# Performance work log

Measured on AMD Instinct MI355X. Metric: run time of the kernel, lower is better.

Reference implementation:

```python
import jax, jax.numpy as jnp
import numpy as np

R, K, CF, HF, WF = 64, 81, 256, 256, 256  # ROIs, classes(incl bg), FPN channels, P2 size
IMG = 1024.0
SCALE = 0.25          # P2 feature stride 4
STEPS = 4             # subdivision steps: 7 -> 112
NPTS = 28 * 28        # subdivision_num_points
FC = 256


def _grid_sample(img, coords):
    """torch.grid_sample(bilinear, align_corners=False, zeros padding).
    img: [N,C,H,W]; coords: [N,P,2] (x,y) in [0,1]. Returns [N,C,P]."""
    N, C, H, W = img.shape
    x = coords[..., 0] * W - 0.5
    y = coords[..., 1] * H - 0.5
    x0 = jnp.floor(x); y0 = jnp.floor(y)
    fx = x - x0; fy = y - y0

    def g(ix, iy, w):
        valid = (ix >= 0) & (ix < W) & (iy >= 0) & (iy < H)
        ixc = jnp.clip(ix, 0, W - 1).astype(jnp.int32)
        iyc = jnp.clip(iy, 0, H - 1).astype(jnp.int32)
        v = jax.vmap(lambda im, yy, xx: im[:, yy, xx])(img, iyc, ixc)  # [N,C,P]
        return v * (w * valid)[:, None, :]

    return (g(x0, y0, (1 - fx) * (1 - fy)) + g(x0 + 1, y0, fx * (1 - fy))
            + g(x0, y0 + 1, (1 - fx) * fy) + g(x0 + 1, y0 + 1, fx * fy))


def _point_head(fine, coarse, W1, b1, W2, b2, W3, b3, Wp, bp):
    # StandardPointHead: 1x1-conv fc layers, coarse logits re-concatenated each layer
    x = jnp.concatenate([fine, coarse], axis=1)  # [R, CF+K, P]
    for Wl, bl in ((W1, b1), (W2, b2), (W3, b3)):
        x = jax.nn.relu(jnp.einsum('oc,rcp->rop', Wl, x) + bl[None, :, None])
        x = jnp.concatenate([x, coarse], axis=1)
    return jnp.einsum('oc,rcp->rop', Wp, x) + bp[None, :, None]  # [R,K,P]


def setup_inputs() -> dict:
    key = jax.random.key(0)
    ks = jax.random.split(key, 12)
    feat = jax.random.normal(ks[0], (1, CF, HF, WF), dtype=jnp.float32)
    u = jax.random.uniform(ks[1], (R, 4), dtype=jnp.float32)
    x0 = u[:, 0] * (IMG - 256.0); y0 = u[:, 1] * (IMG - 256.0)
    w = 32.0 + u[:, 2] * 224.0;   h = 32.0 + u[:, 3] * 224.0
    det_bboxes = jnp.stack([x0, y0, x0 + w, y0 + h], axis=1)
    det_labels = jax.random.randint(ks[2], (R,), 0, 80, dtype=jnp.int32)
    coarse_logits = jax.random.normal(ks[3], (R, K, 7, 7), dtype=jnp.float32)
    cin = CF + K  # = FC + K = 337 for all layers here
    s = 0.02
    return {
        'feat': feat, 'det_bboxes': det_bboxes, 'det_labels': det_labels,
        'coarse_logits': coarse_logits,
        'W1': jax.random.normal(ks[4], (FC, cin), jnp.float32) * s,
        'b1': jnp.zeros((FC,), jnp.float32),
        'W2': jax.random.normal(ks[5], (FC, FC + K), jnp.float32) * s,
        'b2': jnp.zeros((FC,), jnp.float32),
        'W3': jax.random.normal(ks[6], (FC, FC + K), jnp.float32) * s,
        'b3': jnp.zeros((FC,), jnp.float32),
        'Wp': jax.random.normal(ks[7], (K, FC + K), jnp.float32) * s,
        'bp': jnp.zeros((K,), jnp.float32),
    }


def reference(feat, det_bboxes, det_labels, coarse_logits,
              W1, b1, W2, b2, W3, b3, Wp, bp):
    ml = coarse_logits
    bx0, by0 = det_bboxes[:, 0], det_bboxes[:, 1]
    bw = det_bboxes[:, 2] - det_bboxes[:, 0]
    bh = det_bboxes[:, 3] - det_bboxes[:, 1]
    for step in range(STEPS):
        _, _, H, W = ml.shape
        H, W = 2 * H, 2 * W
        # bilinear x2, align_corners=False (half-pixel centers)
        ml = jax.image.resize(ml, (R, K, H, W), method='linear')
        if NPTS >= 4 * H * W and step < STEPS - 1:
            continue
        # uncertainty = -|logit of gt class| (det_labels+1 skips background ch 0)
        gt = ml[jnp.arange(R), det_labels + 1]              # [R,H,W]
        unc = -jnp.abs(gt).reshape(R, H * W)
        _, idx = jax.lax.top_k(unc, NPTS)                   # [R,NPTS]
        px = ((idx % W).astype(ml.dtype) + 0.5) / W
        py = ((idx // W).astype(ml.dtype) + 0.5) / H
        coords = jnp.stack([px, py], axis=-1)               # [R,NPTS,2] in ROI [0,1]
        # project ROI coords to image, then to P2 normalized coords
        cx = bx0[:, None] + coords[..., 0] * bw[:, None]
        cy = by0[:, None] + coords[..., 1] * bh[:, None]
        fcoords = jnp.stack([cx * SCALE / WF, cy * SCALE / HF], axis=-1)
        fine = _grid_sample(feat, fcoords.reshape(1, R * NPTS, 2))  # [1,CF,R*NPTS]
        fine = fine[0].reshape(CF, R, NPTS).transpose(1, 0, 2)      # [R,CF,NPTS]
        coarse = _grid_sample(coarse_logits, coords)                # [R,K,NPTS]
        pl = _point_head(fine, coarse, W1, b1, W2, b2, W3, b3, Wp, bp)
        ml = jax.vmap(lambda m, i, p: m.at[:, i].set(p))(
            ml.reshape(R, K, H * W), idx, pl).reshape(R, K, H, W)
    return ml
```

## Files before the change

kernel.cpp:

```cpp
#include <hip/hip_runtime.h>
#include <hip/hip_bf16.h>
#include <cstdint>
#include <cstddef>

#define R_ 64
#define K_ 81
#define NPTS_ 784

typedef __attribute__((ext_vector_type(8))) short short8;
typedef __attribute__((ext_vector_type(4))) float f32x4;

#define GLDS16(G, L)                                                           \
  __builtin_amdgcn_global_load_lds(                                            \
      (__attribute__((address_space(1))) void*)(void*)(G),                     \
      (__attribute__((address_space(3))) void*)(L), 16, 0, 0)

__global__ __launch_bounds__(256) void transpose_feat_kernel(const float* __restrict__ in,
                                                             float* __restrict__ out) {
  __shared__ float tile[32][33];
  int y = blockIdx.z;
  int x0 = blockIdx.x * 32, c0 = blockIdx.y * 32;
  int tx = threadIdx.x, ty = threadIdx.y;
#pragma unroll
  for (int j = 0; j < 32; j += 8)
    tile[ty + j][tx] = in[(size_t)(c0 + ty + j) * 65536 + (size_t)y * 256 + x0 + tx];
  __syncthreads();
#pragma unroll
  for (int j = 0; j < 32; j += 8)
    out[((size_t)y * 256 + (x0 + ty + j)) * 256 + c0 + tx] = tile[tx][ty + j];
}

__global__ void prep_all_kernel(const float* __restrict__ W1, const float* __restrict__ W2,
                                const float* __restrict__ W3, const float* __restrict__ Wp,
                                const float* __restrict__ b1, const float* __restrict__ b2,
                                const float* __restrict__ b3, const float* __restrict__ bp,
                                const float* __restrict__ coarse_in,
                                __hip_bfloat16* __restrict__ Wpk, float* __restrict__ bias_all,
                                float* __restrict__ coarseT) {
  int t = blockIdx.x * 256 + threadIdx.x;
  if (t < 90112) {
    int lane = t & 63;
    int t2 = t >> 6;
    int hl = t2 & 1;
    t2 >>= 1;
    int jg = t2 & 15;
    t2 >>= 4;
    int kt = t2 % 11;
    int L = t2 / 11;
    int o = jg * 16 + (lane & 15);
    int kbase = kt * 32 + (lane >> 4) * 8;
    const float* Wsrc = (L == 0) ? W1 : (L == 1) ? W2 : (L == 2) ? W3 : Wp;
    int Omax = (L == 3) ? 81 : 256;
    __hip_bfloat16 outv[8];
#pragma unroll
    for (int e = 0; e < 8; ++e) {
      int k = kbase + e;
      float v = (o < Omax && k < 337) ? Wsrc[o * 337 + k] : 0.f;
      __hip_bfloat16 h = __float2bfloat16(v);
      outv[e] = hl ? __float2bfloat16(v - __bfloat162float(h)) : h;
    }
    *(short8*)(Wpk + (size_t)t * 8) = *(const short8*)outv;
  } else if (t < 90112 + 1024) {
    int k = t - 90112;
    float v = 0.f;
    if (k < 256) v = b1[k];
    else if (k < 512) v = b2[k - 256];
    else if (k < 768) v = b3[k - 512];
    else if (k < 768 + 81) v = bp[k - 768];
    bias_all[k] = v;
  } else {
    int t2 = t - 91136;
    if (t2 < R_ * 49 * K_) {
      int k = t2 % K_;
      int t3 = t2 / K_;
      int pos = t3 % 49;
      int r = t3 / 49;
      coarseT[t2] = coarse_in[((size_t)r * K_ + k) * 49 + pos];
    }
  }
}

__global__ __launch_bounds__(128) void upsample2x_kernel(const float* __restrict__ in,
                                                         float* __restrict__ out,
                                                         int Hin, int Win) {
  int b = blockIdx.z;
  int iy = blockIdx.y * 2 + threadIdx.y;
  int ix = blockIdx.x * 64 + threadIdx.x;
  if (ix >= Win || iy >= Hin) return;
  const float* p = in + (size_t)b * Hin * Win;
  int rT = (iy == 0) ? 0 : iy - 1;
  int rB = (iy == Hin - 1) ? iy : iy + 1;
  int cL = (ix == 0) ? 0 : ix - 1;
  int cR = (ix == Win - 1) ? ix : ix + 1;
  float wyT1 = (iy == 0) ? 0.f : 0.75f;
  float wyB1 = (iy == Hin - 1) ? 0.f : 0.25f;
  float wxE1 = (ix == 0) ? 0.f : 0.75f;
  float wxO1 = (ix == Win - 1) ? 0.f : 0.25f;
  float wyT0 = 1.f - wyT1, wyB0 = 1.f - wyB1;
  float wxE0 = 1.f - wxE1, wxO0 = 1.f - wxO1;

  const float* rowA = p + (size_t)rT * Win;
  const float* rowM = p + (size_t)iy * Win;
  const float* rowC = p + (size_t)rB * Win;
  float al = rowA[cL], am = rowA[ix], ar = rowA[cR];
  float mL = rowM[cL], mm = rowM[ix], mr = rowM[cR];
  float cl = rowC[cL], cm = rowC[ix], cr = rowC[cR];

  float aE = wxE0 * al + wxE1 * am;
  float aO = wxO0 * am + wxO1 * ar;
  float mE = wxE0 * mL + wxE1 * mm;
  float mO = wxO0 * mm + wxO1 * mr;
  float cE = wxE0 * cl + wxE1 * cm;
  float cO = wxO0 * cm + wxO1 * cr;

  float oTE = wyT0 * aE + wyT1 * mE;
  float oTO = wyT0 * aO + wyT1 * mO;
  float oBE = wyB0 * mE + wyB1 * cE;
  float oBO = wyB0 * mO + wyB1 * cO;

  int Wout = 2 * Win;
  float* ob = out + ((size_t)b * (2 * Hin) + 2 * iy) * Wout + 2 * ix;
  *(float2*)ob = make_float2(oTE, oTO);
  *(float2*)(ob + Wout) = make_float2(oBE, oBO);
}

__global__ __launch_bounds__(1024) void topk_kernel(const float* __restrict__ ml,
                                                    const int* __restrict__ labels,
                                                    int N, int* __restrict__ sel) {
  int r = blockIdx.x;
  const float* gt = ml + ((size_t)r * K_ + (labels[r] + 1)) * N;
  __shared__ unsigned int hist[256];
  __shared__ unsigned int sh_prefix, sh_remaining, sh_countless;
  __shared__ unsigned int wtot_less[16], wtot_eq[16];
  const int tid = threadIdx.x;
  const int lane = tid & 63;
  const int wv = tid >> 6;

  unsigned int prefix = 0;
  unsigned int remaining = NPTS_;
  unsigned int count_less = 0;
  for (int pass = 0; pass < 4; ++pass) {
    int shift = 24 - 8 * pass;
    if (tid < 256) hist[tid] = 0;
    __syncthreads();
    for (int i = tid; i < N; i += 1024) {
      unsigned int v = __float_as_uint(fabsf(gt[i]));
      bool match = (pass == 0) || ((v >> (shift + 8)) == prefix);
      unsigned int dg = (v >> shift) & 255u;
      if (pass == 0) {
        bool active = match;
        while (true) {
          unsigned long long act = __ballot(active);
          if (!act) break;
          int leader = (int)(__ffsll((long long)act) - 1);
          unsigned int ld = __shfl(dg, leader);
          bool same = active && (dg == ld);
          unsigned long long sm = __ballot(same);
          if (lane == leader) atomicAdd(&hist[ld], (unsigned int)__popcll(sm));
          active = active && !same;
        }
      } else if (match) {
        atomicAdd(&hist[dg], 1u);
      }
    }
    __syncthreads();
    if (tid < 64) {
      unsigned int s0 = hist[4 * lane + 0], s1 = hist[4 * lane + 1];
      unsigned int s2 = hist[4 * lane + 2], s3 = hist[4 * lane + 3];
      unsigned int ls = s0 + s1 + s2 + s3;
      unsigned int inc = ls;
#pragma unroll
      for (int d = 1; d < 64; d <<= 1) {
        unsigned int tv = __shfl_up(inc, d);
        if (lane >= d) inc += tv;
      }
      unsigned int exc = inc - ls;
      bool cross = (exc < remaining) && (exc + ls >= remaining);
      if (cross) {
        unsigned int before = exc;
        int d = 4 * lane;
        if (before + s0 < remaining) {
          before += s0; d++;
          if (before + s1 < remaining) {
            before += s1; d++;
            if (before + s2 < remaining) { before += s2; d++; }
          }
        }
        sh_prefix = (prefix << 8) | (unsigned int)d;
        sh_remaining = remaining - before;
        sh_countless = count_less + before;
      }
    }
    __syncthreads();
    prefix = sh_prefix;
    remaining = sh_remaining;
    count_less = sh_countless;
    __syncthreads();
  }
  unsigned int vstar = prefix;
  unsigned int need_eq = NPTS_ - count_less;

  unsigned int base_less = 0, base_eq = 0;
  int* selr = sel + (size_t)r * NPTS_;
  for (int base = 0; base < N; base += 1024) {
    int i = base + tid;
    bool less = false, eq = false;
    if (i < N) {
      unsigned int v = __float_as_uint(fabsf(gt[i]));
      less = v < vstar;
      eq = v == vstar;
    }
    unsigned long long ml_ = __ballot(less);
    unsigned long long me_ = __ballot(eq);
    unsigned long long lanemask = (lane == 0) ? 0ull : ((~0ull) >> (64 - lane));
    unsigned int pl = __popcll(ml_ & lanemask);
    unsigned int pe = __popcll(me_ & lanemask);
    if (lane == 0) {
      wtot_less[wv] = (unsigned int)__popcll(ml_);
      wtot_eq[wv] = (unsigned int)__popcll(me_);
    }
    __syncthreads();
    unsigned int off_l = 0, off_e = 0, tot_l = 0, tot_e = 0;
#pragma unroll
    for (int w2 = 0; w2 < 16; ++w2) {
      unsigned int tl = wtot_less[w2], te = wtot_eq[w2];
      if (w2 < wv) { off_l += tl; off_e += te; }
      tot_l += tl;
      tot_e += te;
    }
    if (less) selr[base_less + off_l + pl] = i;
    if (eq) {
      unsigned int er = base_eq + off_e + pe;
      if (er < need_eq) selr[count_less + er] = i;
    }
    base_less += tot_l;
    base_eq += tot_e;
    __syncthreads();
  }
}

__global__ __launch_bounds__(256) void sample_kernel(const int* __restrict__ sel,
                                                     const float* __restrict__ bboxes,
                                                     const float* __restrict__ featT,
                                                     const float* __restrict__ coarseT,
                                                     __hip_bfloat16* __restrict__ Xh,
                                                     __hip_bfloat16* __restrict__ Xl,
                                                     __hip_bfloat16* __restrict__ Cth,
                                                     __hip_bfloat16* __restrict__ Ctl,
                                                     int Wlev, int Hlev) {
  int rp = blockIdx.x;
  int r = rp / NPTS_;
  int idx = sel ? sel[rp] : (rp % NPTS_);
  int tid = threadIdx.x;

  float px = ((float)(idx % Wlev) + 0.5f) / (float)Wlev;
  float py = ((float)(idx / Wlev) + 0.5f) / (float)Hlev;
  float bx0 = bboxes[r * 4 + 0], by0 = bboxes[r * 4 + 1];
  float bw = __fsub_rn(bboxes[r * 4 + 2], bx0);
  float bh = __fsub_rn(bboxes[r * 4 + 3], by0);
  float cx = __fadd_rn(bx0, __fmul_rn(px, bw));
  float cy = __fadd_rn(by0, __fmul_rn(py, bh));

  {
    float gx = __fsub_rn(__fmul_rn(cx, 0.25f), 0.5f);
    float gy = __fsub_rn(__fmul_rn(cy, 0.25f), 0.5f);
    float fxf = floorf(gx), fyf = floorf(gy);
    float fx = __fsub_rn(gx, fxf), fy = __fsub_rn(gy, fyf);
    int x0 = (int)fxf, y0 = (int)fyf;
    float ofx = __fsub_rn(1.f, fx), ofy = __fsub_rn(1.f, fy);
    float w00 = __fmul_rn(ofx, ofy);
    float w10 = __fmul_rn(fx, ofy);
    float w01 = __fmul_rn(ofx, fy);
    float w11 = __fmul_rn(fx, fy);
    bool vx0 = (x0 >= 0) && (x0 < 256), vx1 = (x0 + 1 >= 0) && (x0 + 1 < 256);
    bool vy0 = (y0 >= 0) && (y0 < 256), vy1 = (y0 + 1 >= 0) && (y0 + 1 < 256);
    float W00 = (vx0 && vy0) ? w00 : 0.f;
    float W10 = (vx1 && vy0) ? w10 : 0.f;
    float W01 = (vx0 && vy1) ? w01 : 0.f;
    float W11 = (vx1 && vy1) ? w11 : 0.f;
    int x0c = min(max(x0, 0), 255), x1c = min(max(x0 + 1, 0), 255);
    int y0c = min(max(y0, 0), 255), y1c = min(max(y0 + 1, 0), 255);
    const float* p00 = featT + ((size_t)(y0c * 256 + x0c)) * 256;
    const float* p10 = featT + ((size_t)(y0c * 256 + x1c)) * 256;
    const float* p01 = featT + ((size_t)(y1c * 256 + x0c)) * 256;
    const float* p11 = featT + ((size_t)(y1c * 256 + x1c)) * 256;
    float acc = __fmul_rn(p00[tid], W00);
    acc = __fadd_rn(acc, __fmul_rn(p10[tid], W10));
    acc = __fadd_rn(acc, __fmul_rn(p01[tid], W01));
    acc = __fadd_rn(acc, __fmul_rn(p11[tid], W11));
    __hip_bfloat16 h = __float2bfloat16(acc);
    Xh[(size_t)rp * 256 + tid] = h;
    Xl[(size_t)rp * 256 + tid] = __float2bfloat16(acc - __bfloat162float(h));
  }

  if (tid < 96) {
    float acc = 0.f;
    if (tid < K_) {
      float gx = __fsub_rn(__fmul_rn(px, 7.f), 0.5f);
      float gy = __fsub_rn(__fmul_rn(py, 7.f), 0.5f);
      float fxf = floorf(gx), fyf = floorf(gy);
      float fx = __fsub_rn(gx, fxf), fy = __fsub_rn(gy, fyf);
      int x0 = (int)fxf, y0 = (int)fyf;
      float ofx = __fsub_rn(1.f, fx), ofy = __fsub_rn(1.f, fy);
      float w00 = __fmul_rn(ofx, ofy);
      float w10 = __fmul_rn(fx, ofy);
      float w01 = __fmul_rn(ofx, fy);
      float w11 = __fmul_rn(fx, fy);
      bool vx0 = (x0 >= 0) && (x0 < 7), vx1 = (x0 + 1 >= 0) && (x0 + 1 < 7);
      bool vy0 = (y0 >= 0) && (y0 < 7), vy1 = (y0 + 1 >= 0) && (y0 + 1 < 7);
      float W00 = (vx0 && vy0) ? w00 : 0.f;
      float W10 = (vx1 && vy0) ? w10 : 0.f;
      float W01 = (vx0 && vy1) ? w01 : 0.f;
      float W11 = (vx1 && vy1) ? w11 : 0.f;
      int x0c = min(max(x0, 0), 6), x1c = min(max(x0 + 1, 0), 6);
      int y0c = min(max(y0, 0), 6), y1c = min(max(y0 + 1, 0), 6);
      const float* cb = coarseT + (size_t)r * 49 * K_;
      acc = __fmul_rn(cb[(size_t)(y0c * 7 + x0c) * K_ + tid], W00);
      acc = __fadd_rn(acc, __fmul_rn(cb[(size_t)(y0c * 7 + x1c) * K_ + tid], W10));
      acc = __fadd_rn(acc, __fmul_rn(cb[(size_t)(y1c * 7 + x0c) * K_ + tid], W01));
      acc = __fadd_rn(acc, __fmul_rn(cb[(size_t)(y1c * 7 + x1c) * K_ + tid], W11));
    }
    __hip_bfloat16 h = __float2bfloat16(acc);
    Cth[(size_t)rp * 96 + tid] = h;
    Ctl[(size_t)rp * 96 + tid] = __float2bfloat16(acc - __bfloat162float(h));
  }
}

template <int TERMS>
__global__ __launch_bounds__(256, 2) void fused_head_kernel(
    const __hip_bfloat16* __restrict__ Ah, const __hip_bfloat16* __restrict__ Al,
    const __hip_bfloat16* __restrict__ Th, const __hip_bfloat16* __restrict__ Tl,
    const __hip_bfloat16* __restrict__ Wpk,
    const float* __restrict__ bias_all, float* __restrict__ PL) {
  constexpr int XPLANE = 11 * 4096;
  constexpr int XLO = 8 * 4096;
  __shared__ char lds[(TERMS == 3) ? XPLANE + XLO : XPLANE];
  char* Xh = lds;
  char* Xl = lds + XPLANE;

  const int tid = threadIdx.x;
  const int lane = tid & 63;
  const int w = tid >> 6;
  const int g = lane >> 4;
  const int lane15 = lane & 15;
  const int m0 = blockIdx.x * 64;

  {
    const int srow = tid >> 2;
    const int sp = tid & 3;
    const int sx = sp ^ ((srow >> 1) & 3);
#pragma unroll
    for (int kt = 0; kt < 8; ++kt) {
      size_t off = (((size_t)(m0 + srow)) * 256 + (size_t)kt * 32 + (size_t)sx * 8) * 2;
      GLDS16((const char*)Ah + off, Xh + kt * 4096 + w * 1024);
      if constexpr (TERMS == 3) GLDS16((const char*)Al + off, Xl + kt * 4096 + w * 1024);
    }
#pragma unroll
    for (int kt = 8; kt < 11; ++kt) {
      size_t off = (((size_t)(m0 + srow)) * 96 + (size_t)(kt - 8) * 32 + (size_t)sx * 8) * 2;
      GLDS16((const char*)Th + off, Xh + kt * 4096 + w * 1024);
    }
  }
  asm volatile("s_waitcnt vmcnt(0)" ::: "memory");
  __syncthreads();

  int offA[4];
#pragma unroll
  for (int i = 0; i < 4; ++i) {
    int rowA = i * 16 + lane15;
    offA[i] = rowA * 64 + ((g ^ ((rowA >> 1) & 3)) << 4);
  }

#pragma unroll 1
  for (int L = 0; L < 4; ++L) {
    if (L == 3 && w >= 2) break;
    const __hip_bfloat16* WL = Wpk + (size_t)L * (11 * 16 * 2 * 512);

    f32x4 acc[4][4];
#pragma unroll
    for (int i = 0; i < 4; ++i)
#pragma unroll
      for (int j = 0; j < 4; ++j) acc[i][j] = (f32x4){0.f, 0.f, 0.f, 0.f};

    short8 a_h[4], a_l[4], b_h[2][4], b_l[2][4], tl_buf[2][4];

    auto loadB = [&](int buf, int kt) {
#pragma unroll
      for (int j = 0; j < 4; ++j) {
        const __hip_bfloat16* bp =
            WL + (((size_t)kt * 16 + (w * 4 + j)) * 2) * 512 + (size_t)lane * 8;
        b_h[buf][j] = *(const short8*)bp;
        if constexpr (TERMS == 3) b_l[buf][j] = *(const short8*)(bp + 512);
      }
    };
    auto loadTl = [&](int buf, int kt) {
#pragma unroll
      for (int i = 0; i < 4; ++i)
        tl_buf[buf][i] = *(const short8*)((const char*)Tl +
            (((size_t)(m0 + i * 16 + lane15)) * 96 + (size_t)(kt - 8) * 32 +
             (size_t)g * 8) * 2);
    };

    loadB(0, 0);

#pragma unroll
    for (int kt = 0; kt < 11; ++kt) {
      const int cb = kt & 1;
      if (kt < 10) {
        loadB(cb ^ 1, kt + 1);
        if constexpr (TERMS == 3) {
          if (kt + 1 >= 8) loadTl((kt + 1) & 1, kt + 1);
        }
      }
      __builtin_amdgcn_sched_barrier(0);
#pragma unroll
      for (int i = 0; i < 4; ++i) {
        a_h[i] = *(const short8*)(Xh + kt * 4096 + offA[i]);
        if constexpr (TERMS == 3) {
          if (kt < 8)
            a_l[i] = *(const short8*)(Xl + kt * 4096 + offA[i]);
          else
            a_l[i] = tl_buf[kt & 1][i];
        }
      }
      __builtin_amdgcn_s_setprio(1);
#pragma unroll
      for (int i = 0; i < 4; ++i)
#pragma unroll
        for (int j = 0; j < 4; ++j) {
          acc[i][j] = __builtin_amdgcn_mfma_f32_16x16x32_bf16(a_h[i], b_h[cb][j], acc[i][j], 0, 0, 0);
          if constexpr (TERMS == 3) {
            acc[i][j] = __builtin_amdgcn_mfma_f32_16x16x32_bf16(a_h[i], b_l[cb][j], acc[i][j], 0, 0, 0);
            acc[i][j] = __builtin_amdgcn_mfma_f32_16x16x32_bf16(a_l[i], b_h[cb][j], acc[i][j], 0, 0, 0);
          }
        }
      __builtin_amdgcn_s_setprio(0);
      __builtin_amdgcn_sched_barrier(0);
    }

    if (L < 3) {
      __syncthreads();
#pragma unroll
      for (int j = 0; j < 4; ++j) {
        int o = w * 64 + j * 16 + lane15;
        float bv = bias_all[L * 256 + o];
        int kch = o >> 5;
        int s0 = (o >> 3) & 3;
        int e = o & 7;
#pragma unroll
        for (int i = 0; i < 4; ++i) {
          int mb = i * 16 + g * 4;
#pragma unroll
          for (int r = 0; r < 4; ++r) {
            int m = mb + r;
            float v = fmaxf(acc[i][j][r] + bv, 0.f);
            __hip_bfloat16 h = __float2bfloat16(v);
            int boff = kch * 4096 + m * 64 + ((s0 ^ ((m >> 1) & 3)) << 4) + e * 2;
            *(__hip_bfloat16*)(Xh + boff) = h;
            if constexpr (TERMS == 3)
              *(__hip_bfloat16*)(Xl + boff) = __float2bfloat16(v - __bfloat162float(h));
          }
        }
      }
      __syncthreads();
    } else {
#pragma unroll
      for (int j = 0; j < 4; ++j) {
        int o = w * 64 + j * 16 + lane15;
        float bv = bias_all[768 + o];
#pragma unroll
        for (int i = 0; i < 4; ++i) {
          int mb = i * 16 + g * 4;
#pragma unroll
          for (int r = 0; r < 4; ++r)
            PL[(size_t)(m0 + mb + r) * 128 + o] = acc[i][j][r] + bv;
        }
      }
    }
  }
}

__global__ void scatter_kernel(const float* __restrict__ PL, const int* __restrict__ sel,
                               float* __restrict__ ml, int Nlev) {
  int t = blockIdx.x * 256 + threadIdx.x;
  if (t >= R_ * NPTS_ * K_) return;
  int k = t % K_;
  int rp = t / K_;
  int i = sel ? sel[rp] : (rp % NPTS_);
  int r = rp / NPTS_;
  ml[((size_t)r * K_ + k) * Nlev + i] = PL[(size_t)rp * 128 + k];
}

extern "C" void kernel_launch(void* const* d_in, const int* in_sizes, int n_in,
                              void* d_out, int out_size, void* d_ws, size_t ws_size,
                              hipStream_t stream) {
  (void)in_sizes; (void)n_in; (void)out_size; (void)ws_size;
  const float* feat = (const float*)d_in[0];
  const float* bboxes = (const float*)d_in[1];
  const int* labels = (const int*)d_in[2];
  const float* coarse = (const float*)d_in[3];
  const float* W1 = (const float*)d_in[4];
  const float* b1 = (const float*)d_in[5];
  const float* W2 = (const float*)d_in[6];
  const float* b2 = (const float*)d_in[7];
  const float* W3 = (const float*)d_in[8];
  const float* b3 = (const float*)d_in[9];
  const float* Wp = (const float*)d_in[10];
  const float* bp = (const float*)d_in[11];
  float* out = (float*)d_out;

  char* p = (char*)d_ws;
  auto alloc = [&](size_t bytes) { char* r = p; p += (bytes + 255) & ~(size_t)255; return r; };
  float* featT = (float*)alloc(16777216ull * 4);
  float* coarseT = (float*)alloc(254016ull * 4);
  float* ml14 = (float*)alloc(1016064ull * 4);
  float* ml28 = (float*)alloc(4064256ull * 4);
  float* ml56 = (float*)alloc(16257024ull * 4);
  float* PL = (float*)alloc(6422528ull * 4);
  int* sel = (int*)alloc(50176ull * 4);
  __hip_bfloat16* Xa_h = (__hip_bfloat16*)alloc(12845056ull * 2);
  __hip_bfloat16* Xa_l = (__hip_bfloat16*)alloc(12845056ull * 2);
  __hip_bfloat16* Ct_h = (__hip_bfloat16*)alloc(4816896ull * 2);
  __hip_bfloat16* Ct_l = (__hip_bfloat16*)alloc(4816896ull * 2);
  __hip_bfloat16* Wpk = (__hip_bfloat16*)alloc(720896ull * 2);
  float* bias_all = (float*)alloc(1024ull * 4);

  const int N = R_ * NPTS_;
  const int B = R_ * K_;

  transpose_feat_kernel<<<dim3(8, 8, 256), dim3(32, 8), 0, stream>>>(feat, featT);
  prep_all_kernel<<<1349, 256, 0, stream>>>(W1, W2, W3, Wp, b1, b2, b3, bp, coarse, Wpk, bias_all, coarseT);

  upsample2x_kernel<<<dim3(1, 4, B), dim3(64, 2), 0, stream>>>(coarse, ml14, 7, 7);

  upsample2x_kernel<<<dim3(1, 7, B), dim3(64, 2), 0, stream>>>(ml14, ml28, 14, 14);
  sample_kernel<<<N, 256, 0, stream>>>(nullptr, bboxes, featT, coarseT, Xa_h, Xa_l, Ct_h, Ct_l, 28, 28);
  fused_head_kernel<3><<<784, 256, 0, stream>>>(Xa_h, Xa_l, Ct_h, Ct_l, Wpk, bias_all, PL);
  scatter_kernel<<<15876, 256, 0, stream>>>(PL, nullptr, ml28, 784);

  upsample2x_kernel<<<dim3(1, 14, B), dim3(64, 2), 0, stream>>>(ml28, ml56, 28, 28);
  topk_kernel<<<R_, 1024, 0, stream>>>(ml56, labels, 3136, sel);
  sample_kernel<<<N, 256, 0, stream>>>(sel, bboxes, featT, coarseT, Xa_h, Xa_l, Ct_h, Ct_l, 56, 56);
  fused_head_kernel<3><<<784, 256, 0, stream>>>(Xa_h, Xa_l, Ct_h, Ct_l, Wpk, bias_all, PL);
  scatter_kernel<<<15876, 256, 0, stream>>>(PL, sel, ml56, 3136);

  upsample2x_kernel<<<dim3(1, 28, B), dim3(64, 2), 0, stream>>>(ml56, out, 56, 56);
  topk_kernel<<<R_, 1024, 0, stream>>>(out, labels, 12544, sel);
  sample_kernel<<<N, 256, 0, stream>>>(sel, bboxes, featT, coarseT, Xa_h, Xa_l, Ct_h, Ct_l, 112, 112);
  fused_head_kernel<1><<<784, 256, 0, stream>>>(Xa_h, nullptr, Ct_h, nullptr, Wpk, bias_all, PL);
  scatter_kernel<<<15876, 256, 0, stream>>>(PL, sel, out, 12544);
}
```

Measured before the change: 831.4 us.

## Skip redundant early upsamples and fuse final scatter into last upsample

```diff
diff --git a/kernel.cpp b/kernel.cpp
--- a/kernel.cpp
+++ b/kernel.cpp
@@ -80,14 +80,9 @@
   }
 }
 
-__global__ __launch_bounds__(128) void upsample2x_kernel(const float* __restrict__ in,
-                                                         float* __restrict__ out,
-                                                         int Hin, int Win) {
-  int b = blockIdx.z;
-  int iy = blockIdx.y * 2 + threadIdx.y;
-  int ix = blockIdx.x * 64 + threadIdx.x;
-  if (ix >= Win || iy >= Hin) return;
-  const float* p = in + (size_t)b * Hin * Win;
+__device__ __forceinline__ void quad_upsample(const float* __restrict__ p, int Hin, int Win,
+                                              int iy, int ix, float& oTE, float& oTO,
+                                              float& oBE, float& oBO) {
   int rT = (iy == 0) ? 0 : iy - 1;
   int rB = (iy == Hin - 1) ? iy : iy + 1;
   int cL = (ix == 0) ? 0 : ix - 1;
@@ -98,37 +93,100 @@
   float wxO1 = (ix == Win - 1) ? 0.f : 0.25f;
   float wyT0 = 1.f - wyT1, wyB0 = 1.f - wyB1;
   float wxE0 = 1.f - wxE1, wxO0 = 1.f - wxO1;
-
   const float* rowA = p + (size_t)rT * Win;
   const float* rowM = p + (size_t)iy * Win;
   const float* rowC = p + (size_t)rB * Win;
   float al = rowA[cL], am = rowA[ix], ar = rowA[cR];
   float mL = rowM[cL], mm = rowM[ix], mr = rowM[cR];
   float cl = rowC[cL], cm = rowC[ix], cr = rowC[cR];
-
   float aE = wxE0 * al + wxE1 * am;
   float aO = wxO0 * am + wxO1 * ar;
   float mE = wxE0 * mL + wxE1 * mm;
   float mO = wxO0 * mm + wxO1 * mr;
   float cE = wxE0 * cl + wxE1 * cm;
   float cO = wxO0 * cm + wxO1 * cr;
-
-  float oTE = wyT0 * aE + wyT1 * mE;
-  float oTO = wyT0 * aO + wyT1 * mO;
-  float oBE = wyB0 * mE + wyB1 * cE;
-  float oBO = wyB0 * mO + wyB1 * cO;
-
+  oTE = wyT0 * aE + wyT1 * mE;
+  oTO = wyT0 * aO + wyT1 * mO;
+  oBE = wyB0 * mE + wyB1 * cE;
+  oBO = wyB0 * mO + wyB1 * cO;
+}
+
+__global__ __launch_bounds__(128) void upsample2x_kernel(const float* __restrict__ in,
+                                                         float* __restrict__ out,
+                                                         int Hin, int Win) {
+  int b = blockIdx.z;
+  int iy = blockIdx.y * 2 + threadIdx.y;
+  int ix = blockIdx.x * 64 + threadIdx.x;
+  if (ix >= Win || iy >= Hin) return;
+  const float* p = in + (size_t)b * Hin * Win;
+  float oTE, oTO, oBE, oBO;
+  quad_upsample(p, Hin, Win, iy, ix, oTE, oTO, oBE, oBO);
   int Wout = 2 * Win;
   float* ob = out + ((size_t)b * (2 * Hin) + 2 * iy) * Wout + 2 * ix;
   *(float2*)ob = make_float2(oTE, oTO);
   *(float2*)(ob + Wout) = make_float2(oBE, oBO);
 }
 
+__global__ __launch_bounds__(128) void upsample2x_gt_kernel(const float* __restrict__ ml56,
+                                                            const int* __restrict__ labels,
+                                                            float* __restrict__ gtbuf) {
+  int r = blockIdx.z;
+  int iy = blockIdx.y * 2 + threadIdx.y;
+  int ix = blockIdx.x * 64 + threadIdx.x;
+  if (ix >= 56 || iy >= 56) return;
+  const float* p = ml56 + ((size_t)r * K_ + (labels[r] + 1)) * 3136;
+  float oTE, oTO, oBE, oBO;
+  quad_upsample(p, 56, 56, iy, ix, oTE, oTO, oBE, oBO);
+  float* ob = gtbuf + ((size_t)r * 112 + 2 * iy) * 112 + 2 * ix;
+  *(float2*)ob = make_float2(oTE, oTO);
+  *(float2*)(ob + 112) = make_float2(oBE, oBO);
+}
+
+__global__ __launch_bounds__(128) void upsample2x_sel_kernel(const float* __restrict__ ml56,
+                                                             const unsigned short* __restrict__ map,
+                                                             const float* __restrict__ PL,
+                                                             float* __restrict__ out) {
+  int b = blockIdx.z;
+  int r = b / K_;
+  int k = b - r * K_;
+  int iy = blockIdx.y * 2 + threadIdx.y;
+  int ix = blockIdx.x * 64 + threadIdx.x;
+  if (ix >= 56 || iy >= 56) return;
+  const float* p = ml56 + (size_t)b * 3136;
+  float oTE, oTO, oBE, oBO;
+  quad_upsample(p, 56, 56, iy, ix, oTE, oTO, oBE, oBO);
+  int oy = 2 * iy, ox = 2 * ix;
+  const unsigned short* mr = map + (size_t)r * 12544;
+  unsigned short r0 = mr[oy * 112 + ox], r1 = mr[oy * 112 + ox + 1];
+  unsigned short r2 = mr[(oy + 1) * 112 + ox], r3 = mr[(oy + 1) * 112 + ox + 1];
+  if (r0 != 0xFFFFu) oTE = PL[((size_t)r * NPTS_ + r0) * 128 + k];
+  if (r1 != 0xFFFFu) oTO = PL[((size_t)r * NPTS_ + r1) * 128 + k];
+  if (r2 != 0xFFFFu) oBE = PL[((size_t)r * NPTS_ + r2) * 128 + k];
+  if (r3 != 0xFFFFu) oBO = PL[((size_t)r * NPTS_ + r3) * 128 + k];
+  float* ob = out + ((size_t)b * 112 + oy) * 112 + ox;
+  *(float2*)ob = make_float2(oTE, oTO);
+  *(float2*)(ob + 112) = make_float2(oBE, oBO);
+}
+
+__global__ void mapinit_kernel(unsigned short* __restrict__ map) {
+  int t = blockIdx.x * 256 + threadIdx.x;
+  if (t < R_ * 12544) map[t] = 0xFFFFu;
+}
+__global__ void mapbuild_kernel(const int* __restrict__ sel, unsigned short* __restrict__ map) {
+  int t = blockIdx.x * 256 + threadIdx.x;
+  if (t < R_ * NPTS_) {
+    int r = t / NPTS_;
+    map[(size_t)r * 12544 + sel[t]] = (unsigned short)(t % NPTS_);
+  }
+}
+
 __global__ __launch_bounds__(1024) void topk_kernel(const float* __restrict__ ml,
                                                     const int* __restrict__ labels,
+                                                    const float* __restrict__ gtdirect,
                                                     int N, int* __restrict__ sel) {
   int r = blockIdx.x;
-  const float* gt = ml + ((size_t)r * K_ + (labels[r] + 1)) * N;
+  const float* gt = gtdirect ? (gtdirect + (size_t)r * N)
+                             : (ml + ((size_t)r * K_ + (labels[r] + 1)) * N);
   __shared__ unsigned int hist[256];
   __shared__ unsigned int sh_prefix, sh_remaining, sh_countless;
   __shared__ unsigned int wtot_less[16], wtot_eq[16];
@@ -513,11 +571,12 @@
   auto alloc = [&](size_t bytes) { char* r = p; p += (bytes + 255) & ~(size_t)255; return r; };
   float* featT = (float*)alloc(16777216ull * 4);
   float* coarseT = (float*)alloc(254016ull * 4);
-  float* ml14 = (float*)alloc(1016064ull * 4);
   float* ml28 = (float*)alloc(4064256ull * 4);
   float* ml56 = (float*)alloc(16257024ull * 4);
   float* PL = (float*)alloc(6422528ull * 4);
   int* sel = (int*)alloc(50176ull * 4);
+  float* gtbuf = (float*)alloc(802816ull * 4);
+  unsigned short* map = (unsigned short*)alloc(802816ull * 2);
   __hip_bfloat16* Xa_h = (__hip_bfloat16*)alloc(12845056ull * 2);
   __hip_bfloat16* Xa_l = (__hip_bfloat16*)alloc(12845056ull * 2);
   __hip_bfloat16* Ct_h = (__hip_bfloat16*)alloc(4816896ull * 2);
@@ -530,23 +589,22 @@
 
   transpose_feat_kernel<<<dim3(8, 8, 256), dim3(32, 8), 0, stream>>>(feat, featT);
   prep_all_kernel<<<1349, 256, 0, stream>>>(W1, W2, W3, Wp, b1, b2, b3, bp, coarse, Wpk, bias_all, coarseT);
-
-  upsample2x_kernel<<<dim3(1, 4, B), dim3(64, 2), 0, stream>>>(coarse, ml14, 7, 7);
-
-  upsample2x_kernel<<<dim3(1, 7, B), dim3(64, 2), 0, stream>>>(ml14, ml28, 14, 14);
+  mapinit_kernel<<<3136, 256, 0, stream>>>(map);
+
   sample_kernel<<<N, 256, 0, stream>>>(nullptr, bboxes, featT, coarseT, Xa_h, Xa_l, Ct_h, Ct_l, 28, 28);
   fused_head_kernel<3><<<784, 256, 0, stream>>>(Xa_h, Xa_l, Ct_h, Ct_l, Wpk, bias_all, PL);
   scatter_kernel<<<15876, 256, 0, stream>>>(PL, nullptr, ml28, 784);
 
   upsample2x_kernel<<<dim3(1, 14, B), dim3(64, 2), 0, stream>>>(ml28, ml56, 28, 28);
-  topk_kernel<<<R_, 1024, 0, stream>>>(ml56, labels, 3136, sel);
+  topk_kernel<<<R_, 1024, 0, stream>>>(ml56, labels, nullptr, 3136, sel);
   sample_kernel<<<N, 256, 0, stream>>>(sel, bboxes, featT, coarseT, Xa_h, Xa_l, Ct_h, Ct_l, 56, 56);
   fused_head_kernel<3><<<784, 256, 0, stream>>>(Xa_h, Xa_l, Ct_h, Ct_l, Wpk, bias_all, PL);
   scatter_kernel<<<15876, 256, 0, stream>>>(PL, sel, ml56, 3136);
 
-  upsample2x_kernel<<<dim3(1, 28, B), dim3(64, 2), 0, stream>>>(ml56, out, 56, 56);
-  topk_kernel<<<R_, 1024, 0, stream>>>(out, labels, 12544, sel);
+  upsample2x_gt_kernel<<<dim3(1, 28, R_), dim3(64, 2), 0, stream>>>(ml56, labels, gtbuf);
+  topk_kernel<<<R_, 1024, 0, stream>>>(nullptr, labels, gtbuf, 12544, sel);
   sample_kernel<<<N, 256, 0, stream>>>(sel, bboxes, featT, coarseT, Xa_h, Xa_l, Ct_h, Ct_l, 112, 112);
   fused_head_kernel<1><<<784, 256, 0, stream>>>(Xa_h, nullptr, Ct_h, nullptr, Wpk, bias_all, PL);
-  scatter_kernel<<<15876, 256, 0, stream>>>(PL, sel, out, 12544);
-}
+  mapbuild_kernel<<<196, 256, 0, stream>>>(sel, map);
+  upsample2x_sel_kernel<<<dim3(1, 28, B), dim3(64, 2), 0, stream>>>(ml56, map, PL, out);
+}
```

New measurement: 763.9 us. 8.1% less time.
